# Kernel tuning notes

Hardware: AMD Instinct MI355X
Metric: run time of the kernel (lower is better)

The kernel has to match this reference:

```python
import jax, jax.numpy as jnp
import numpy as np

N_NODES = 100000
IN_DIM = 500
HID = 64
N_CLASSES = 47
N_EDGES = 1200000
K_LAYERS = 2


def _spmm_rownorm(edge_index, h, n):
    # Row-normalized D^{-1} A @ h via gather + segment_sum over edge list.
    src, dst = edge_index[0], edge_index[1]
    ones = jnp.ones(src.shape[0], dtype=h.dtype)
    deg = jax.ops.segment_sum(ones, src, num_segments=n)
    inv_deg = 1.0 / jnp.maximum(deg, 1.0)
    msg = h[dst] * inv_deg[src][:, None]  # [E, HID]
    return jax.ops.segment_sum(msg, src, num_segments=n)  # [N, HID]


def setup_inputs() -> dict:
    key = jax.random.key(0)
    ks = jax.random.split(key, 12)
    x = jax.random.normal(ks[0], (N_NODES, IN_DIM), dtype=jnp.float32)
    edge_index_1 = jax.random.randint(ks[1], (2, N_EDGES), 0, N_NODES, dtype=jnp.int32)
    edge_index_2 = jax.random.randint(ks[2], (2, N_EDGES), 0, N_NODES, dtype=jnp.int32)
    s = 0.02
    W_embed = jax.random.normal(ks[3], (IN_DIM, HID), dtype=jnp.float32) * s
    b_embed = jnp.zeros((HID,), dtype=jnp.float32)
    W0 = jax.random.normal(ks[4], (4 * HID, HID), dtype=jnp.float32) * s
    b0 = jnp.zeros((HID,), dtype=jnp.float32)
    W1 = jax.random.normal(ks[5], (4 * HID, HID), dtype=jnp.float32) * s
    b1 = jnp.zeros((HID,), dtype=jnp.float32)
    Wc = jax.random.normal(ks[6], (HID * (K_LAYERS + 1), N_CLASSES), dtype=jnp.float32) * s
    bc = jnp.zeros((N_CLASSES,), dtype=jnp.float32)
    return {"x": x, "edge_index_1": edge_index_1, "edge_index_2": edge_index_2,
            "W_embed": W_embed, "b_embed": b_embed, "W0": W0, "b0": b0,
            "W1": W1, "b1": b1, "Wc": Wc, "bc": bc}


def reference(x, edge_index_1, edge_index_2, W_embed, b_embed, W0, b0, W1, b1, Wc, bc):
    n = x.shape[0]
    r0 = jax.nn.relu(x @ W_embed + b_embed)  # dropout = identity in eval
    reps = [r0]
    r_prev = r0
    for (W, b) in ((W0, b0), (W1, b1)):
        n1 = _spmm_rownorm(edge_index_1, r_prev, n)
        n2 = _spmm_rownorm(edge_index_2, r_prev, n)
        concat = jnp.concatenate([r_prev, n1, r_prev, n2], axis=1)  # ego separation
        r_k = jax.nn.relu(concat @ W + b)
        reps.append(r_k)
        r_prev = r_k
    emb = jnp.concatenate(reps, axis=1)  # [N, HID*(K+1)]
    logits = emb @ Wc + bc
    return logits
```

## Files before the change

kernel.cpp:

```cpp
#include <hip/hip_runtime.h>

namespace {

constexpr int N  = 100000;
constexpr int KD = 500;
constexpr int E  = 1200000;
constexpr int NC = 47;

constexpr int M2  = 2 * N;
constexpr int E2  = 2 * E;
constexpr int NB  = 391;
constexpr int AB  = 586;
constexpr int EBMAX = 8192;

typedef __attribute__((ext_vector_type(8))) short short8;
typedef __attribute__((ext_vector_type(4))) float f32x4;

__device__ __forceinline__ ushort f2bf(float f) {
    union { float f; uint u; } c; c.f = f;
    uint u = c.u + 0x7fffu + ((c.u >> 16) & 1);
    return (ushort)(u >> 16);
}
__device__ __forceinline__ float bflo(uint v) { union { uint u; float f; } c; c.u = v << 16;        return c.f; }
__device__ __forceinline__ float bfhi(uint v) { union { uint u; float f; } c; c.u = v & 0xffff0000u; return c.f; }


__global__ __launch_bounds__(256) void prep_all(const float* __restrict__ We, const float* __restrict__ W0,
                                                const float* __restrict__ W1, const float* __restrict__ Wc,
                                                const float* __restrict__ bc,
                                                int* __restrict__ cursor, ushort* __restrict__ wtE,
                                                ushort* __restrict__ wf0, ushort* __restrict__ wf1,
                                                ushort* __restrict__ wct, float* __restrict__ bcp) {
    int i = blockIdx.x * 256 + threadIdx.x;
    if (i < NB) cursor[i] = i * EBMAX;
    if (i < 64 * 512) {
        int c = i >> 9, k = i & 511;
        wtE[i] = f2bf(k < KD ? We[k * 64 + c] : 0.f);
    }
    if (i < 64 * 192) {
        int c = i / 192, k = i % 192;
        float v0, v1;
        if (k < 64)       { v0 = W0[k * 64 + c] + W0[(128 + k) * 64 + c];
                            v1 = W1[k * 64 + c] + W1[(128 + k) * 64 + c]; }
        else if (k < 128) { v0 = W0[k * 64 + c]; v1 = W1[k * 64 + c]; }
        else              { v0 = W0[(k + 64) * 64 + c]; v1 = W1[(k + 64) * 64 + c]; }
        wf0[i] = f2bf(v0);
        wf1[i] = f2bf(v1);
        wct[i] = f2bf(c < NC ? Wc[k * NC + c] : 0.f);
    }
    if (i < 64) bcp[i] = (i < NC) ? bc[i] : 0.f;
}


__global__ __launch_bounds__(256) void bucket_scatter(const int* __restrict__ src1, const int* __restrict__ dst1,
                                                      const int* __restrict__ src2, const int* __restrict__ dst2,
                                                      int* __restrict__ cursor, uint* __restrict__ ebuf) {
    __shared__ int h[NB];
    __shared__ int claim[NB];
    int t = threadIdx.x;
    int mb[16];
    uint mu[16];
    for (int b = t; b < NB; b += 256) h[b] = 0;
    __syncthreads();
    #pragma unroll
    for (int q = 0; q < 16; ++q) {
        int i = blockIdx.x * 4096 + q * 256 + t;
        if (i < E2) {
            int g = i >= E;
            int idx = i - g * E;
            int s = g ? src2[idx] : src1[idx];
            int d = g ? dst2[idx] : dst1[idx];
            int v = g * N + s;
            mb[q] = v >> 9;
            mu[q] = ((uint)(v & 511) << 17) | (uint)d;
            atomicAdd(&h[mb[q]], 1);
        } else {
            mb[q] = -1;
            mu[q] = 0;
        }
    }
    __syncthreads();
    for (int b = t; b < NB; b += 256)
        claim[b] = h[b] ? atomicAdd(&cursor[b], h[b]) : 0;
    __syncthreads();
    for (int b = t; b < NB; b += 256) h[b] = 0;
    __syncthreads();
    #pragma unroll
    for (int q = 0; q < 16; ++q) {
        if (mb[q] >= 0) {
            int r = atomicAdd(&h[mb[q]], 1);
            ebuf[claim[mb[q]] + r] = mu[q];
        }
    }
}

__global__ __launch_bounds__(256) void csr_finalize(const uint* __restrict__ ebuf, const int* __restrict__ cursor,
                                                    int* __restrict__ rp, int* __restrict__ rpe,
                                                    float* __restrict__ invd, int* __restrict__ col) {
    __shared__ uint eb[EBMAX];
    __shared__ int h[512];
    __shared__ int ex[512];
    __shared__ int ps[256];
    int bid = blockIdx.x;
    int t = threadIdx.x;
    int b0 = bid * EBMAX;
    int cnt = cursor[bid] - b0;
    if (cnt > EBMAX) cnt = EBMAX;
    if (cnt < 0) cnt = 0;
    h[t] = 0; h[t + 256] = 0;
    for (int j = t; j < cnt; j += 256) eb[j] = ebuf[b0 + j];
    __syncthreads();
    for (int j = t; j < cnt; j += 256) atomicAdd(&h[eb[j] >> 17], 1);
    __syncthreads();
    int pv = h[2 * t] + h[2 * t + 1];
    ps[t] = pv;
    __syncthreads();
    for (int off = 1; off < 256; off <<= 1) {
        int x = (t >= off) ? ps[t - off] : 0;
        __syncthreads();
        ps[t] += x;
        __syncthreads();
    }
    int e2 = ps[t] - pv;
    ex[2 * t] = e2;
    ex[2 * t + 1] = e2 + h[2 * t];
    __syncthreads();
    #pragma unroll
    for (int q = 0; q < 2; ++q) {
        int k = q * 256 + t;
        int n = bid * 512 + k;
        if (n < M2) {
            int st = b0 + ex[k];
            int dv = h[k];
            rp[n]  = st;
            rpe[n] = st + dv;
            invd[n] = 1.0f / (float)(dv > 1 ? dv : 1);
        }
    }
    __syncthreads();
    for (int j = t; j < cnt; j += 256) {
        uint u = eb[j];
        int ls = u >> 17;
        int r = atomicAdd(&ex[ls], 1);
        col[b0 + r] = (int)(u & 0x1FFFFu) * 384;
    }
}


__device__ __forceinline__ void stageB(const ushort* __restrict__ Wt, int ldw, int k0, short* Bs) {
    const int tid = threadIdx.x;
    #pragma unroll
    for (int i = 0; i < 2; ++i) {
        int idx = tid + i * 256;
        int c = idx >> 3, qc = (idx & 7) * 8;
        uint4 v = *reinterpret_cast<const uint4*>(Wt + (size_t)c * ldw + k0 + qc);
        *reinterpret_cast<uint4*>(Bs + (((c << 6) + qc) ^ ((c & 7) << 3))) = v;
    }
}

__device__ __forceinline__ void mma64(const short* As, const short* Bs, f32x4 acc[2][4]) {
    const int lane = threadIdx.x & 63;
    const int wrow = (threadIdx.x >> 6) * 32;
    const int llo = lane & 15, lhi = lane >> 4;
    #pragma unroll
    for (int kf = 0; kf < 2; ++kf) {
        const int kb = kf * 32 + lhi * 8;
        short8 a[2], b[4];
        #pragma unroll
        for (int m = 0; m < 2; ++m) {
            int r = wrow + m * 16 + llo;
            a[m] = *reinterpret_cast<const short8*>(As + (((r << 6) + kb) ^ ((r & 7) << 3)));
        }
        #pragma unroll
        for (int n = 0; n < 4; ++n) {
            int c = n * 16 + llo;
            b[n] = *reinterpret_cast<const short8*>(Bs + (((c << 6) + kb) ^ ((c & 7) << 3)));
        }
        #pragma unroll
        for (int m = 0; m < 2; ++m)
            #pragma unroll
            for (int n = 0; n < 4; ++n)
                acc[m][n] = __builtin_amdgcn_mfma_f32_16x16x32_bf16(a[m], b[n], acc[m][n], 0, 0, 0);
    }
}

template<bool OUTF32>
__device__ __forceinline__ void epilogue(f32x4 acc[2][4], const float* __restrict__ bias,
                                         void* out, int ldo, int ocols, int relu, int rbase) {
    const int lane = threadIdx.x & 63;
    const int wrow = (threadIdx.x >> 6) * 32;
    #pragma unroll
    for (int m = 0; m < 2; ++m) {
        #pragma unroll
        for (int r = 0; r < 4; ++r) {
            int orow = rbase + wrow + m * 16 + (lane >> 4) * 4 + r;
            if (orow >= N) continue;
            #pragma unroll
            for (int n = 0; n < 4; ++n) {
                int c = n * 16 + (lane & 15);
                float v = acc[m][n][r] + bias[c];
                if (relu) v = fmaxf(v, 0.f);
                if (OUTF32) {
                    if (c < ocols) ((float*)out)[(size_t)orow * ldo + c] = v;
                } else {
                    ((ushort*)out)[(size_t)orow * ldo + c] = f2bf(v);
                }
            }
        }
    }
}

__global__ __launch_bounds__(256) void gemm_embed(const float* __restrict__ x,
                                                  const ushort* __restrict__ WtE,
                                                  const float* __restrict__ bias,
                                                  ushort* __restrict__ out) {
    __shared__ short As[128 * 64];
    __shared__ short Bs[64 * 64];
    const int tid = threadIdx.x;
    const int rbase = blockIdx.x * 128;
    f32x4 acc[2][4] = {};
    for (int k0 = 0; k0 < 512; k0 += 64) {
        __syncthreads();
        #pragma unroll
        for (int i = 0; i < 8; ++i) {
            int idx = tid + i * 256;
            int r = idx >> 4, qc = (idx & 15) * 4;
            int grow = rbase + r;
            float4 v = {0.f, 0.f, 0.f, 0.f};
            if (grow < N && k0 + qc < KD) v = *reinterpret_cast<const float4*>(x + (size_t)grow * KD + k0 + qc);
            uint2 p;
            p.x = (uint)f2bf(v.x) | ((uint)f2bf(v.y) << 16);
            p.y = (uint)f2bf(v.z) | ((uint)f2bf(v.w) << 16);
            *reinterpret_cast<uint2*>(As + (((r << 6) + qc) ^ ((r & 7) << 3))) = p;
        }
        stageB(WtE, 512, k0, Bs);
        __syncthreads();
        mma64(As, Bs, acc);
    }
    epilogue<false>(acc, bias, out, 192, 64, 1, rbase);
}

template<bool OUTF32>
__global__ __launch_bounds__(256) void gemm3(const ushort* __restrict__ a0, int lda0,
                                             const ushort* __restrict__ a1, int lda1,
                                             const ushort* __restrict__ a2, int lda2,
                                             const ushort* __restrict__ Wt,
                                             const float* __restrict__ bias,
                                             void* out, int ldo, int ocols, int relu) {
    __shared__ short As[128 * 64];
    __shared__ short Bs[64 * 64];
    const int tid = threadIdx.x;
    const int rbase = blockIdx.x * 128;
    f32x4 acc[2][4] = {};
    const ushort* aseg[3] = {a0, a1, a2};
    const int ldas[3] = {lda0, lda1, lda2};
    #pragma unroll
    for (int seg = 0; seg < 3; ++seg) {
        const ushort* A = aseg[seg];
        const int lda = ldas[seg];
        __syncthreads();
        #pragma unroll
        for (int i = 0; i < 4; ++i) {
            int idx = tid + i * 256;
            int r = idx >> 3, qc = (idx & 7) * 8;
            int grow = rbase + r;
            uint4 v = {0u, 0u, 0u, 0u};
            if (grow < N) v = *reinterpret_cast<const uint4*>(A + (size_t)grow * lda + qc);
            *reinterpret_cast<uint4*>(As + (((r << 6) + qc) ^ ((r & 7) << 3))) = v;
        }
        stageB(Wt, 192, seg * 64, Bs);
        __syncthreads();
        mma64(As, Bs, acc);
    }
    epilogue<OUTF32>(acc, bias, out, ldo, ocols, relu, rbase);
}


__global__ __launch_bounds__(256) void spmm7(const int* __restrict__ rp, const int* __restrict__ rpe,
                                             const int* __restrict__ col,
                                             const float* __restrict__ invd,
                                             const ushort* __restrict__ table, int colOff,
                                             ushort* __restrict__ n1b, ushort* __restrict__ n2b) {
    int gid = (blockIdx.x * 256 + threadIdx.x) >> 3;
    int ls = threadIdx.x & 7;
    if (gid >= M2) return;
    const char* hb = (const char*)(table + colOff) + ls * 16;
    float w = invd[gid];
    int s = rp[gid], e = rpe[gid];
    int e1 = e - 1;
    float a0=0.f,a1=0.f,a2=0.f,a3=0.f,a4=0.f,a5=0.f,a6=0.f,a7=0.f;
    for (int j = s; j < e; j += 8) {
        int off[8];
        float wv[8];
        #pragma unroll
        for (int u = 0; u < 8; ++u) {
            int jj = j + u;
            int cidx = jj < e ? jj : e1;
            off[u] = col[cidx];
            wv[u] = jj < e ? 1.f : 0.f;
        }
        uint4 v[8];
        #pragma unroll
        for (int u = 0; u < 8; ++u) v[u] = *reinterpret_cast<const uint4*>(hb + off[u]);
        #pragma unroll
        for (int u = 0; u < 8; ++u) {
            a0 = fmaf(wv[u], bflo(v[u].x), a0); a1 = fmaf(wv[u], bfhi(v[u].x), a1);
            a2 = fmaf(wv[u], bflo(v[u].y), a2); a3 = fmaf(wv[u], bfhi(v[u].y), a3);
            a4 = fmaf(wv[u], bflo(v[u].z), a4); a5 = fmaf(wv[u], bfhi(v[u].z), a5);
            a6 = fmaf(wv[u], bflo(v[u].w), a6); a7 = fmaf(wv[u], bfhi(v[u].w), a7);
        }
    }
    int g = gid >= N;
    int node = gid - g * N;
    ushort* op = g ? n2b : n1b;
    uint4 o;
    o.x = (uint)f2bf(a0 * w) | ((uint)f2bf(a1 * w) << 16);
    o.y = (uint)f2bf(a2 * w) | ((uint)f2bf(a3 * w) << 16);
    o.z = (uint)f2bf(a4 * w) | ((uint)f2bf(a5 * w) << 16);
    o.w = (uint)f2bf(a6 * w) | ((uint)f2bf(a7 * w) << 16);
    *reinterpret_cast<uint4*>(op + (size_t)node * 64 + ls * 8) = o;
}

}

extern "C" void kernel_launch(void* const* d_in, const int* in_sizes, int n_in,
                              void* d_out, int out_size, void* d_ws, size_t ws_size,
                              hipStream_t stream) {
    const float* x       = (const float*)d_in[0];
    const int*   ei1     = (const int*)d_in[1];
    const int*   ei2     = (const int*)d_in[2];
    const float* W_embed = (const float*)d_in[3];
    const float* b_embed = (const float*)d_in[4];
    const float* W0      = (const float*)d_in[5];
    const float* b0      = (const float*)d_in[6];
    const float* W1      = (const float*)d_in[7];
    const float* b1      = (const float*)d_in[8];
    const float* Wc      = (const float*)d_in[9];
    const float* bc      = (const float*)d_in[10];
    float* out = (float*)d_out;

    char* ws = (char*)d_ws;
    size_t off = 0;
    auto alloc = [&](size_t bytes) -> void* {
        void* p = ws + off;
        off += (bytes + 255) & ~(size_t)255;
        return p;
    };

    ushort* embB  = (ushort*)alloc((size_t)N * 192 * 2);
    ushort* n1b   = (ushort*)alloc((size_t)N * 64 * 2);
    ushort* n2b   = (ushort*)alloc((size_t)N * 64 * 2);
    int*    col   = (int*)alloc((size_t)NB * EBMAX * 4);
    uint*   ebuf  = (uint*)alloc((size_t)NB * EBMAX * 4);
    int*    rp    = (int*)alloc((size_t)M2 * 4);
    int*    rpe   = (int*)alloc((size_t)M2 * 4);
    float*  invd  = (float*)alloc((size_t)M2 * 4);
    int*    bcur  = (int*)alloc((NB + 1) * 4);
    ushort* wtE   = (ushort*)alloc(64 * 512 * 2);
    ushort* weff0 = (ushort*)alloc(64 * 192 * 2);
    ushort* weff1 = (ushort*)alloc(64 * 192 * 2);
    ushort* wct   = (ushort*)alloc(64 * 192 * 2);
    float*  bcp   = (float*)alloc(64 * 4);
    if (off > ws_size) return;

    const int* src1 = ei1, *dst1 = ei1 + E;
    const int* src2 = ei2, *dst2 = ei2 + E;

    const int GB = (N + 127) / 128;
    const int PB = (M2 * 8 + 255) / 256;

    prep_all<<<128, 256, 0, stream>>>(W_embed, W0, W1, Wc, bc, bcur, wtE, weff0, weff1, wct, bcp);

    bucket_scatter<<<AB, 256, 0, stream>>>(src1, dst1, src2, dst2, bcur, ebuf);
    csr_finalize<<<NB, 256, 0, stream>>>(ebuf, bcur, rp, rpe, invd, col);

    gemm_embed<<<GB, 256, 0, stream>>>(x, wtE, b_embed, embB);

    for (int layer = 0; layer < 2; ++layer) {
        const ushort* rprev = embB + 64 * layer;
        spmm7<<<PB, 256, 0, stream>>>(rp, rpe, col, invd, embB, 64 * layer, n1b, n2b);
        const ushort* Wl = (layer == 0) ? weff0 : weff1;
        const float*  bl = (layer == 0) ? b0 : b1;
        gemm3<false><<<GB, 256, 0, stream>>>(rprev, 192, n1b, 64, n2b, 64, Wl, bl,
                                             embB + 64 * (layer + 1), 192, 64, 1);
    }

    gemm3<true><<<GB, 256, 0, stream>>>(embB, 192, embB + 64, 192, embB + 128, 192, wct, bcp,
                                        out, NC, NC, 0);
}
```

Before: 231.0 us.

## Retile embed GEMM to 32-row blocks with full-K A prefetch into LDS

The embedding GEMM now uses 32-row tiles instead of 128, launching N/32 blocks. Each thread issues all 16 float4 loads of its row segment up front and converts them to bf16 into a full-K LDS tile before the K loop. The loop then only stages B, and each wave computes a 16-column slice with 16x16x32 MFMAs. The aim is more blocks and more loads in flight to better saturate bandwidth on the 200MB x read, at the cost of more B restaging across blocks and more registers per thread.

After: 223.6 us. 1.03x faster.

```diff
diff --git a/kernel.cpp b/kernel.cpp
--- a/kernel.cpp
+++ b/kernel.cpp
@@ -116,9 +116,9 @@
     ps[t] = pv;
     __syncthreads();
     for (int off = 1; off < 256; off <<= 1) {
-        int x = (t >= off) ? ps[t - off] : 0;
-        __syncthreads();
-        ps[t] += x;
+        int xv = (t >= off) ? ps[t - off] : 0;
+        __syncthreads();
+        ps[t] += xv;
         __syncthreads();
     }
     int e2 = ps[t] - pv;
@@ -210,34 +210,76 @@
     }
 }
 
+
 __global__ __launch_bounds__(256) void gemm_embed(const float* __restrict__ x,
                                                   const ushort* __restrict__ WtE,
                                                   const float* __restrict__ bias,
                                                   ushort* __restrict__ out) {
-    __shared__ short As[128 * 64];
+    __shared__ short As[32 * 512];
     __shared__ short Bs[64 * 64];
     const int tid = threadIdx.x;
-    const int rbase = blockIdx.x * 128;
-    f32x4 acc[2][4] = {};
+    const int rbase = blockIdx.x * 32;
+    const int r = tid >> 3;
+    const int j = tid & 7;
+    const int swz = (r & 7) << 3;
+
+    const float* xrow = x + (size_t)(rbase + r) * KD;
+    float4 pv[16];
+    #pragma unroll
+    for (int i = 0; i < 16; ++i) {
+        int qc = i * 32 + j * 4;
+        float4 v = {0.f, 0.f, 0.f, 0.f};
+        if (qc < KD) v = *reinterpret_cast<const float4*>(xrow + qc);
+        pv[i] = v;
+    }
+    #pragma unroll
+    for (int i = 0; i < 16; ++i) {
+        int qc = i * 32 + j * 4;
+        uint2 p;
+        p.x = (uint)f2bf(pv[i].x) | ((uint)f2bf(pv[i].y) << 16);
+        p.y = (uint)f2bf(pv[i].z) | ((uint)f2bf(pv[i].w) << 16);
+        *reinterpret_cast<uint2*>(As + ((r << 9) + (qc ^ swz))) = p;
+    }
+
+    const int lane = tid & 63;
+    const int w = tid >> 6;
+    const int llo = lane & 15, lhi = lane >> 4;
+    f32x4 acc[2] = {};
     for (int k0 = 0; k0 < 512; k0 += 64) {
         __syncthreads();
-        #pragma unroll
-        for (int i = 0; i < 8; ++i) {
-            int idx = tid + i * 256;
-            int r = idx >> 4, qc = (idx & 15) * 4;
-            int grow = rbase + r;
-            float4 v = {0.f, 0.f, 0.f, 0.f};
-            if (grow < N && k0 + qc < KD) v = *reinterpret_cast<const float4*>(x + (size_t)grow * KD + k0 + qc);
-            uint2 p;
-            p.x = (uint)f2bf(v.x) | ((uint)f2bf(v.y) << 16);
-            p.y = (uint)f2bf(v.z) | ((uint)f2bf(v.w) << 16);
-            *reinterpret_cast<uint2*>(As + (((r << 6) + qc) ^ ((r & 7) << 3))) = p;
-        }
         stageB(WtE, 512, k0, Bs);
         __syncthreads();
-        mma64(As, Bs, acc);
-    }
-    epilogue<false>(acc, bias, out, 192, 64, 1, rbase);
+        #pragma unroll
+        for (int kf = 0; kf < 2; ++kf) {
+            const int kbl = kf * 32 + lhi * 8;
+            const int kab = k0 + kbl;
+            short8 a[2], b;
+            #pragma unroll
+            for (int m = 0; m < 2; ++m) {
+                int ar = m * 16 + llo;
+                a[m] = *reinterpret_cast<const short8*>(As + ((ar << 9) + (kab ^ ((ar & 7) << 3))));
+            }
+            {
+                int c = w * 16 + llo;
+                b = *reinterpret_cast<const short8*>(Bs + (((c << 6) + kbl) ^ ((c & 7) << 3)));
+            }
+            #pragma unroll
+            for (int m = 0; m < 2; ++m)
+                acc[m] = __builtin_amdgcn_mfma_f32_16x16x32_bf16(a[m], b, acc[m], 0, 0, 0);
+        }
+    }
+
+    #pragma unroll
+    for (int m = 0; m < 2; ++m) {
+        #pragma unroll
+        for (int rr = 0; rr < 4; ++rr) {
+            int orow = rbase + m * 16 + lhi * 4 + rr;
+            int c = w * 16 + llo;
+            float v = acc[m][rr] + bias[c];
+            v = fmaxf(v, 0.f);
+            out[(size_t)orow * 192 + c] = f2bf(v);
+        }
+    }
 }
 
 template<bool OUTF32>
@@ -366,15 +408,16 @@
     const int* src1 = ei1, *dst1 = ei1 + E;
     const int* src2 = ei2, *dst2 = ei2 + E;
 
-    const int GB = (N + 127) / 128;
-    const int PB = (M2 * 8 + 255) / 256;
+    const int GB  = (N + 127) / 128;
+    const int GBE = N / 32;
+    const int PB  = (M2 * 8 + 255) / 256;
 
     prep_all<<<128, 256, 0, stream>>>(W_embed, W0, W1, Wc, bc, bcur, wtE, weff0, weff1, wct, bcp);
 
     bucket_scatter<<<AB, 256, 0, stream>>>(src1, dst1, src2, dst2, bcur, ebuf);
     csr_finalize<<<NB, 256, 0, stream>>>(ebuf, bcur, rp, rpe, invd, col);
 
-    gemm_embed<<<GB, 256, 0, stream>>>(x, wtE, b_embed, embB);
+    gemm_embed<<<GBE, 256, 0, stream>>>(x, wtE, b_embed, embB);
 
     for (int layer = 0; layer < 2; ++layer) {
         const ushort* rprev = embB + 64 * layer;
```
